# Performance work log

Hardware: AMD Instinct MI355X
Metric: run time of the kernel (lower is better)

The kernel has to match this reference:

```python
import jax, jax.numpy as jnp
import numpy as np

N, IN1, IN2, OUT, DX, DY = 32, 4, 4, 128, 128, 128


def setup_inputs() -> dict:
    key = jax.random.key(0)
    k = jax.random.split(key, 6)
    x = jax.random.normal(k[0], (N, IN1, DX), dtype=jnp.float32)
    y = jax.random.normal(k[1], (N, IN2, DY), dtype=jnp.float32)
    # kernel_C: [out_channels, in1*in2]
    C = jax.random.normal(k[2], (OUT, IN1 * IN2), dtype=jnp.float32) * 0.1
    # one Conv1d pair (kernel_size=3 -> only j=1: k=2, dilation=2, padding=1)
    W_A = jax.random.normal(k[3], (OUT, IN1 * IN2, 2), dtype=jnp.float32) * 0.1
    W_B = jax.random.normal(k[4], (OUT, IN1 * IN2, 2), dtype=jnp.float32) * 0.1
    bias = jax.random.uniform(k[5], (OUT,), dtype=jnp.float32, minval=-0.5, maxval=0.5)
    return {"x": x, "y": y, "C": C, "W_A": W_A, "W_B": W_B, "bias": bias}


def _dilated_conv(inp, w):
    # PyTorch Conv1d(kernel_size=2, stride=1, padding=1, dilation=2, bias=False)
    return jax.lax.conv_general_dilated(
        inp, w, window_strides=(1,), padding=[(1, 1)], rhs_dilation=(2,),
        dimension_numbers=("NCH", "OIH", "NCH"))


def reference(x, y, C, W_A, W_B, bias):
    n, in1, dx = x.shape
    _, in2, dy = y.shape
    out_ch = C.shape[0]
    # batch_cross_product: channel c = c1*in2 + c2 of outer product, then einsum with C.
    # Fused form (same math, no [N, in1*dx, in2*dy] intermediate):
    Cr = C.reshape(out_ch, in1, in2)
    bcp = jnp.einsum("nci,ndj,ocd->noij", x, y, Cr)  # [N, out, dx, dy]
    # x.repeat(1, in2, 1) / y.repeat(1, in1, 1) == tile along channel dim
    xA = jnp.tile(x, (1, in2, 1))  # [N, in1*in2, dx]
    yB = jnp.tile(y, (1, in1, 1))  # [N, in1*in2, dy]
    a = _dilated_conv(xA, W_A)  # [N, out, dx]
    b = _dilated_conv(yB, W_B)  # [N, out, dy]
    out = bcp + a[:, :, :, None] + b[:, :, None, :]
    return out + bias[None, :, None, None]
```

## Files before the change

### kernel.cpp

```cpp
#include <hip/hip_runtime.h>


__global__ __launch_bounds__(256) void scvc_kernel(
    const float* __restrict__ x,
    const float* __restrict__ y,
    const float* __restrict__ C,
    const float* __restrict__ WA,
    const float* __restrict__ WB,
    const float* __restrict__ bias,
    float* __restrict__ out)
{
    const int n   = blockIdx.x >> 7;
    const int o   = blockIdx.x & 127;
    const int tid = threadIdx.x;

    __shared__ float csh[16];
    __shared__ float wash[8];
    __shared__ float wbsh[8];
    __shared__ float t4[128][4];
    __shared__ float arow[128];
    __shared__ float bcol[128];

    const float* xb = x + n * 512;
    const float* yb = y + n * 512;

    if (tid < 16) {
        csh[tid] = C[o * 16 + tid];
    } else if (tid < 24) {
        const int idx = tid - 16;
        const int c = idx >> 1, k = idx & 1;
        float s = 0.f;
        #pragma unroll
        for (int r = 0; r < 4; ++r) s += WA[o * 32 + (4 * r + c) * 2 + k];
        wash[idx] = s;
    } else if (tid < 32) {
        const int idx = tid - 24;
        const int c = idx >> 1, k = idx & 1;
        float s = 0.f;
        #pragma unroll
        for (int r = 0; r < 4; ++r) s += WB[o * 32 + (4 * r + c) * 2 + k];
        wbsh[idx] = s;
    }
    __syncthreads();

    if (tid < 128) {
        const int i = tid;
        float xv[4], xm[4], xp[4];
        #pragma unroll
        for (int c = 0; c < 4; ++c) {
            xv[c] = xb[c * 128 + i];
            xm[c] = (i > 0)   ? xb[c * 128 + i - 1] : 0.f;
            xp[c] = (i < 127) ? xb[c * 128 + i + 1] : 0.f;
        }
        #pragma unroll
        for (int d = 0; d < 4; ++d) {
            float s = 0.f;
            #pragma unroll
            for (int c = 0; c < 4; ++c) s += xv[c] * csh[c * 4 + d];
            t4[i][d] = s;
        }
        float a = 0.f;
        #pragma unroll
        for (int c = 0; c < 4; ++c)
            a += xm[c] * wash[c * 2] + xp[c] * wash[c * 2 + 1];
        arow[i] = a;
    } else {
        const int j = tid - 128;
        float b = bias[o];
        #pragma unroll
        for (int c = 0; c < 4; ++c) {
            float ym = (j > 0)   ? yb[c * 128 + j - 1] : 0.f;
            float yp = (j < 127) ? yb[c * 128 + j + 1] : 0.f;
            b += ym * wbsh[c * 2] + yp * wbsh[c * 2 + 1];
        }
        bcol[j] = b;
    }
    __syncthreads();

    const int col4 = (tid & 31) * 4;
    const int rgrp = tid >> 5;

    float yr[4][4];
    #pragma unroll
    for (int d = 0; d < 4; ++d) {
        const float4 v = *(const float4*)(yb + d * 128 + col4);
        yr[d][0] = v.x; yr[d][1] = v.y; yr[d][2] = v.z; yr[d][3] = v.w;
    }
    float bj[4];
    #pragma unroll
    for (int jj = 0; jj < 4; ++jj) bj[jj] = bcol[col4 + jj];

    float* op = out + ((long)blockIdx.x << 14) + col4;
    #pragma unroll
    for (int it = 0; it < 16; ++it) {
        const int i = rgrp + it * 8;
        const float4 t = *(const float4*)(&t4[i][0]);
        const float ai = arow[i];
        float4 r;
        r.x = t.x * yr[0][0] + t.y * yr[1][0] + t.z * yr[2][0] + t.w * yr[3][0] + (ai + bj[0]);
        r.y = t.x * yr[0][1] + t.y * yr[1][1] + t.z * yr[2][1] + t.w * yr[3][1] + (ai + bj[1]);
        r.z = t.x * yr[0][2] + t.y * yr[1][2] + t.z * yr[2][2] + t.w * yr[3][2] + (ai + bj[2]);
        r.w = t.x * yr[0][3] + t.y * yr[1][3] + t.z * yr[2][3] + t.w * yr[3][3] + (ai + bj[3]);
        *(float4*)(op + i * 128) = r;
    }
}

extern "C" void kernel_launch(void* const* d_in, const int* in_sizes, int n_in,
                              void* d_out, int out_size, void* d_ws, size_t ws_size,
                              hipStream_t stream) {
    const float* x    = (const float*)d_in[0];
    const float* y    = (const float*)d_in[1];
    const float* C    = (const float*)d_in[2];
    const float* WA   = (const float*)d_in[3];
    const float* WB   = (const float*)d_in[4];
    const float* bias = (const float*)d_in[5];
    float* out = (float*)d_out;

    scvc_kernel<<<32 * 128, 256, 0, stream>>>(x, y, C, WA, WB, bias, out);
}
```

Measured before the change: 266.4 us.

## Remap work so each wave handles two rows across all batches

The kernel drops shared memory and both __syncthreads. Each 64-lane wave now owns one output channel and two rows and loops over all 32 batch items. Per-channel weights (C and the summed WA/WB) are loaded into registers once and reused across the batch loop, and the row and column conv terms are recomputed per batch. This removes the per-block setup, the barriers and the redundant weight loads. In exchange, every batch iteration reloads x and y from cache, writes are strided by the batch stride, and the grid is smaller.

Result: slower. 394.0 us (+47.9%).

```diff
diff --git a/kernel.cpp b/kernel.cpp
--- a/kernel.cpp
+++ b/kernel.cpp
@@ -10,98 +10,89 @@
     const float* __restrict__ bias,
     float* __restrict__ out)
 {
-    const int n   = blockIdx.x >> 7;
-    const int o   = blockIdx.x & 127;
-    const int tid = threadIdx.x;
+    const int wg   = (blockIdx.x << 2) + (threadIdx.x >> 6);
+    const int lane = threadIdx.x & 63;
+    const int o    = wg >> 6;
+    const int k    = wg & 63;
+    const int half = lane >> 5;
+    const int i    = (k << 1) + half;
+    const int col4 = (lane & 31) << 2;
 
-    __shared__ float csh[16];
-    __shared__ float wash[8];
-    __shared__ float wbsh[8];
-    __shared__ float t4[128][4];
-    __shared__ float arow[128];
-    __shared__ float bcol[128];
+    float cr[4][4];
+    #pragma unroll
+    for (int c = 0; c < 4; ++c) {
+        #pragma unroll
+        for (int d = 0; d < 4; ++d)
+            cr[c][d] = C[o * 16 + c * 4 + d];
+    }
 
-    const float* xb = x + n * 512;
-    const float* yb = y + n * 512;
+    float wam[4], wap[4], wbm[4], wbp[4];
+    const float mm = (i > 0)   ? 1.f : 0.f;
+    const float mp = (i < 127) ? 1.f : 0.f;
+    #pragma unroll
+    for (int c = 0; c < 4; ++c) {
+        float sa0 = 0.f, sa1 = 0.f, sb0 = 0.f, sb1 = 0.f;
+        #pragma unroll
+        for (int r = 0; r < 4; ++r) {
+            sa0 += WA[o * 32 + (4 * r + c) * 2 + 0];
+            sa1 += WA[o * 32 + (4 * r + c) * 2 + 1];
+            sb0 += WB[o * 32 + (4 * r + c) * 2 + 0];
+            sb1 += WB[o * 32 + (4 * r + c) * 2 + 1];
+        }
+        wam[c] = sa0 * mm;
+        wap[c] = sa1 * mp;
+        wbm[c] = sb0;
+        wbp[c] = sb1;
+    }
+    const float bo = bias[o];
 
-    if (tid < 16) {
-        csh[tid] = C[o * 16 + tid];
-    } else if (tid < 24) {
-        const int idx = tid - 16;
-        const int c = idx >> 1, k = idx & 1;
-        float s = 0.f;
-        #pragma unroll
-        for (int r = 0; r < 4; ++r) s += WA[o * 32 + (4 * r + c) * 2 + k];
-        wash[idx] = s;
-    } else if (tid < 32) {
-        const int idx = tid - 24;
-        const int c = idx >> 1, k = idx & 1;
-        float s = 0.f;
-        #pragma unroll
-        for (int r = 0; r < 4; ++r) s += WB[o * 32 + (4 * r + c) * 2 + k];
-        wbsh[idx] = s;
-    }
-    __syncthreads();
+    const int   im = (i > 0)      ? i - 1    : 0;
+    const int   ip = (i < 127)    ? i + 1    : 0;
+    const float cm = (col4 > 0)   ? 1.f : 0.f;
+    const float cp = (col4 < 124) ? 1.f : 0.f;
+    const int   jm = (col4 > 0)   ? col4 - 1 : 0;
+    const int   jp = (col4 < 124) ? col4 + 4 : 0;
 
-    if (tid < 128) {
-        const int i = tid;
-        float xv[4], xm[4], xp[4];
+    float* op = out + (long)o * 16384 + i * 128 + col4;
+
+    #pragma unroll 2
+    for (int n = 0; n < 32; ++n) {
+        const float* xb = x + (n << 9);
+        const float* yb = y + (n << 9);
+
+        float t40 = 0.f, t41 = 0.f, t42 = 0.f, t43 = 0.f, a = 0.f;
         #pragma unroll
         for (int c = 0; c < 4; ++c) {
-            xv[c] = xb[c * 128 + i];
-            xm[c] = (i > 0)   ? xb[c * 128 + i - 1] : 0.f;
-            xp[c] = (i < 127) ? xb[c * 128 + i + 1] : 0.f;
+            const float xc = xb[(c << 7) + i];
+            t40 = fmaf(xc, cr[c][0], t40);
+            t41 = fmaf(xc, cr[c][1], t41);
+            t42 = fmaf(xc, cr[c][2], t42);
+            t43 = fmaf(xc, cr[c][3], t43);
+            a = fmaf(xb[(c << 7) + im], wam[c], a);
+            a = fmaf(xb[(c << 7) + ip], wap[c], a);
         }
+
+        float bj0 = bo, bj1 = bo, bj2 = bo, bj3 = bo;
+        float yr[4][4];
         #pragma unroll
         for (int d = 0; d < 4; ++d) {
-            float s = 0.f;
-            #pragma unroll
-            for (int c = 0; c < 4; ++c) s += xv[c] * csh[c * 4 + d];
-            t4[i][d] = s;
+            const float4 v = *(const float4*)(yb + (d << 7) + col4);
+            yr[d][0] = v.x; yr[d][1] = v.y; yr[d][2] = v.z; yr[d][3] = v.w;
+            const float ymv = yb[(d << 7) + jm] * cm;
+            const float ypv = yb[(d << 7) + jp] * cp;
+            bj0 = fmaf(ymv, wbm[d], bj0); bj0 = fmaf(v.y, wbp[d], bj0);
+            bj1 = fmaf(v.x, wbm[d], bj1); bj1 = fmaf(v.z, wbp[d], bj1);
+            bj2 = fmaf(v.y, wbm[d], bj2); bj2 = fmaf(v.w, wbp[d], bj2);
+            bj3 = fmaf(v.z, wbm[d], bj3); bj3 = fmaf(ypv, wbp[d], bj3);
         }
-        float a = 0.f;
-        #pragma unroll
-        for (int c = 0; c < 4; ++c)
-            a += xm[c] * wash[c * 2] + xp[c] * wash[c * 2 + 1];
-        arow[i] = a;
-    } else {
-        const int j = tid - 128;
-        float b = bias[o];
-        #pragma unroll
-        for (int c = 0; c < 4; ++c) {
-            float ym = (j > 0)   ? yb[c * 128 + j - 1] : 0.f;
-            float yp = (j < 127) ? yb[c * 128 + j + 1] : 0.f;
-            b += ym * wbsh[c * 2] + yp * wbsh[c * 2 + 1];
-        }
-        bcol[j] = b;
-    }
-    __syncthreads();
 
-    const int col4 = (tid & 31) * 4;
-    const int rgrp = tid >> 5;
-
-    float yr[4][4];
-    #pragma unroll
-    for (int d = 0; d < 4; ++d) {
-        const float4 v = *(const float4*)(yb + d * 128 + col4);
-        yr[d][0] = v.x; yr[d][1] = v.y; yr[d][2] = v.z; yr[d][3] = v.w;
-    }
-    float bj[4];
-    #pragma unroll
-    for (int jj = 0; jj < 4; ++jj) bj[jj] = bcol[col4 + jj];
-
-    float* op = out + ((long)blockIdx.x << 14) + col4;
-    #pragma unroll
-    for (int it = 0; it < 16; ++it) {
-        const int i = rgrp + it * 8;
-        const float4 t = *(const float4*)(&t4[i][0]);
-        const float ai = arow[i];
         float4 r;
-        r.x = t.x * yr[0][0] + t.y * yr[1][0] + t.z * yr[2][0] + t.w * yr[3][0] + (ai + bj[0]);
-        r.y = t.x * yr[0][1] + t.y * yr[1][1] + t.z * yr[2][1] + t.w * yr[3][1] + (ai + bj[1]);
-        r.z = t.x * yr[0][2] + t.y * yr[1][2] + t.z * yr[2][2] + t.w * yr[3][2] + (ai + bj[2]);
-        r.w = t.x * yr[0][3] + t.y * yr[1][3] + t.z * yr[2][3] + t.w * yr[3][3] + (ai + bj[3]);
-        *(float4*)(op + i * 128) = r;
+        r.x = t40 * yr[0][0] + t41 * yr[1][0] + t42 * yr[2][0] + t43 * yr[3][0] + (a + bj0);
+        r.y = t40 * yr[0][1] + t41 * yr[1][1] + t42 * yr[2][1] + t43 * yr[3][1] + (a + bj1);
+        r.z = t40 * yr[0][2] + t41 * yr[1][2] + t42 * yr[2][2] + t43 * yr[3][2] + (a + bj2);
+        r.w = t40 * yr[0][3] + t41 * yr[1][3] + t42 * yr[2][3] + t43 * yr[3][3] + (a + bj3);
+        *(float4*)op = r;
+        op += 2097152;
     }
 }
 
@@ -116,5 +107,5 @@
     const float* bias = (const float*)d_in[5];
     float* out = (float*)d_out;
 
-    scvc_kernel<<<32 * 128, 256, 0, stream>>>(x, y, C, WA, WB, bias, out);
+    scvc_kernel<<<2048, 256, 0, stream>>>(x, y, C, WA, WB, bias, out);
 }
```
